# Kernel optimization log

Measured on AMD Instinct MI355X. Metric: run time of the kernel, lower is better.

The kernel has to match this reference:

```python
import jax, jax.numpy as jnp
import numpy as np

N, DIM = 8192, 128

def setup_inputs() -> dict:
    key = jax.random.key(0)
    ks = jax.random.split(key, 9)
    s = 1.0 / np.sqrt(DIM)
    return {
        "x": jax.random.normal(ks[0], (N, DIM), dtype=jnp.float32),
        "Wq": jax.random.uniform(ks[1], (DIM, DIM), jnp.float32, -s, s),
        "bq": jax.random.uniform(ks[2], (DIM,), jnp.float32, -s, s),
        "Wk": jax.random.uniform(ks[3], (DIM, DIM), jnp.float32, -s, s),
        "bk": jax.random.uniform(ks[4], (DIM,), jnp.float32, -s, s),
        "Wv": jax.random.uniform(ks[5], (DIM, DIM), jnp.float32, -s, s),
        "bv": jax.random.uniform(ks[6], (DIM,), jnp.float32, -s, s),
        "Wo": jax.random.uniform(ks[7], (DIM, DIM), jnp.float32, -s, s),
        "bo": jax.random.uniform(ks[8], (DIM,), jnp.float32, -s, s),
    }

def reference(x, Wq, bq, Wk, bk, Wv, bv, Wo, bo):
    # nn.Linear: y = x @ W.T + b
    Q = x @ Wq.T + bq                      # [N, d]
    K = x @ Wk.T + bk                      # [N, d]
    V = x @ Wv.T + bv                      # [N, d]
    scale = 1.0 / jnp.sqrt(jnp.asarray(x.shape[-1], x.dtype))
    scores = (Q @ K.T) * scale             # [N, N] — matches original O(n^2) math
    attn = jax.nn.softmax(scores, axis=-1)
    out = attn @ V                         # [N, d]
    return out @ Wo.T + bo
```

## Files before the change

### kernel.cpp

```cpp
#include <hip/hip_runtime.h>
#include <math.h>


typedef __bf16 bf16x8 __attribute__((ext_vector_type(8)));
typedef float f32x4 __attribute__((ext_vector_type(4)));
typedef unsigned int u32x4 __attribute__((ext_vector_type(4)));
typedef unsigned int u32x2 __attribute__((ext_vector_type(2)));
typedef unsigned short us16;

#define NTOK 8192
#define CHUNKS 8

static constexpr float SCALE_L2E = 0.08838834764831845f * 1.4426950408889634f;

__device__ __forceinline__ unsigned f2bf_u(float x) {
    unsigned u = __builtin_bit_cast(unsigned, x);
    return (u + 0x7FFFu + ((u >> 16) & 1u)) >> 16;
}

__device__ __forceinline__ unsigned pk_bf16(float x, float y) {
    unsigned a = __builtin_bit_cast(unsigned, x) + 0x8000u;
    unsigned b = __builtin_bit_cast(unsigned, y) + 0x8000u;
#if __has_builtin(__builtin_amdgcn_perm)
    return __builtin_amdgcn_perm(b, a, 0x07060302u);
#else
    return (a >> 16) | (b & 0xFFFF0000u);
#endif
}

__device__ __forceinline__ bf16x8 ld_frag(const us16* p) {
    u32x4 u = *reinterpret_cast<const u32x4*>(p);
    return __builtin_bit_cast(bf16x8, u);
}

__global__ __launch_bounds__(256) void cast_all(
    const float* __restrict__ x,
    const float* __restrict__ wq, const float* __restrict__ wk,
    const float* __restrict__ wv, const float* __restrict__ wo,
    us16* __restrict__ xb,
    us16* __restrict__ wqb, us16* __restrict__ wkb,
    us16* __restrict__ wvb, us16* __restrict__ wob)
{
    int b = blockIdx.x;
    const float* src; us16* dst; int off;
    if (b < 512) { src = x; dst = xb; off = b * 2048; }
    else {
        int wi = (b - 512) >> 3, sb = (b - 512) & 7;
        src = wi == 0 ? wq : wi == 1 ? wk : wi == 2 ? wv : wo;
        dst = wi == 0 ? wqb : wi == 1 ? wkb : wi == 2 ? wvb : wob;
        off = sb * 2048;
    }
    int i = off + threadIdx.x * 8;
    f32x4 a = *reinterpret_cast<const f32x4*>(src + i);
    f32x4 c = *reinterpret_cast<const f32x4*>(src + i + 4);
    u32x4 o;
    o[0] = f2bf_u(a[0]) | (f2bf_u(a[1]) << 16);
    o[1] = f2bf_u(a[2]) | (f2bf_u(a[3]) << 16);
    o[2] = f2bf_u(c[0]) | (f2bf_u(c[1]) << 16);
    o[3] = f2bf_u(c[2]) | (f2bf_u(c[3]) << 16);
    *reinterpret_cast<u32x4*>(dst + i) = o;
}

__global__ __launch_bounds__(256) void proj_qkv(
    const us16* __restrict__ xb,
    const us16* __restrict__ wqb, const float* __restrict__ bq,
    const us16* __restrict__ wkb, const float* __restrict__ bk,
    const us16* __restrict__ wvb, const float* __restrict__ bv,
    us16* __restrict__ Qb, us16* __restrict__ Kb, us16* __restrict__ Vt)
{
    int z = blockIdx.x >> 7;
    int tile = blockIdx.x & 127;
    const us16* W = z == 0 ? wqb : z == 1 ? wkb : wvb;
    const float* bias = z == 0 ? bq : z == 1 ? bk : bv;
    float osc = z == 0 ? SCALE_L2E : 1.0f;

    int w = threadIdx.x >> 6, lane = threadIdx.x & 63;
    int quad = lane >> 4, l15 = lane & 15;
    int rbase = tile * 64 + w * 16;

    bf16x8 af[4];
#pragma unroll
    for (int ks = 0; ks < 4; ++ks)
        af[ks] = ld_frag(xb + (rbase + l15) * 128 + ks * 32 + quad * 8);

    f32x4 acc[8];
#pragma unroll
    for (int nt = 0; nt < 8; ++nt) acc[nt] = f32x4{0.f, 0.f, 0.f, 0.f};

#pragma unroll
    for (int nt = 0; nt < 8; ++nt) {
#pragma unroll
        for (int ks = 0; ks < 4; ++ks) {
            bf16x8 bf = ld_frag(W + (nt * 16 + l15) * 128 + ks * 32 + quad * 8);
            acc[nt] = __builtin_amdgcn_mfma_f32_16x16x32_bf16(af[ks], bf, acc[nt], 0, 0, 0);
        }
    }

#pragma unroll
    for (int nt = 0; nt < 8; ++nt) {
        float bb = bias[nt * 16 + l15];
        if (z < 2) {
            us16* Out = z == 0 ? Qb : Kb;
#pragma unroll
            for (int r = 0; r < 4; ++r)
                Out[(rbase + quad * 4 + r) * 128 + nt * 16 + l15] =
                    (us16)f2bf_u((acc[nt][r] + bb) * osc);
        } else {
            int d = nt * 16 + l15, r0 = rbase + quad * 4;
            u32x2 pk;
            pk[0] = f2bf_u(acc[nt][0] + bb) | (f2bf_u(acc[nt][1] + bb) << 16);
            pk[1] = f2bf_u(acc[nt][2] + bb) | (f2bf_u(acc[nt][3] + bb) << 16);
            *reinterpret_cast<u32x2*>(Vt + d * NTOK + r0) = pk;
        }
    }
}

__global__ __launch_bounds__(256, 2) void attn(
    const us16* __restrict__ Qb, const us16* __restrict__ Kb,
    const us16* __restrict__ Vt,
    float* __restrict__ Opart, float* __restrict__ Lpart)
{
    __shared__ us16 ldsK[64 * 136];
    __shared__ us16 ldsV[128 * 72];
    __shared__ us16 ldsP[4][32 * 72];

    int qtile = blockIdx.x >> 3, chunk = blockIdx.x & 7;
    int tid = threadIdx.x, w = tid >> 6, lane = tid & 63;
    int quad = lane >> 4, l15 = lane & 15;
    int qb0 = qtile * 128 + w * 32;

    bf16x8 qf[2][4];
#pragma unroll
    for (int mt = 0; mt < 2; ++mt)
#pragma unroll
        for (int ks = 0; ks < 4; ++ks)
            qf[mt][ks] = ld_frag(Qb + (qb0 + mt * 16 + l15) * 128 + ks * 32 + quad * 8);

    f32x4 o[2][8];
#pragma unroll
    for (int mt = 0; mt < 2; ++mt)
#pragma unroll
        for (int dt = 0; dt < 8; ++dt) o[mt][dt] = f32x4{0.f, 0.f, 0.f, 0.f};

    f32x4 lacc[2];
    lacc[0] = f32x4{0.f, 0.f, 0.f, 0.f};
    lacc[1] = f32x4{0.f, 0.f, 0.f, 0.f};

    u32x4 onesu;
    onesu[0] = onesu[1] = onesu[2] = onesu[3] = 0x3F803F80u;
    bf16x8 ones = __builtin_bit_cast(bf16x8, onesu);

    us16* pw = &ldsP[w][0];

    for (int it = 0; it < 16; ++it) {
        int kk = chunk * 1024 + it * 64;
#pragma unroll
        for (int c = 0; c < 4; ++c) {
            int idx = tid + c * 256;
            int r = idx >> 4, cc = idx & 15;
            *reinterpret_cast<u32x4*>(ldsK + r * 136 + cc * 8) =
                *reinterpret_cast<const u32x4*>(Kb + (kk + r) * 128 + cc * 8);
        }
#pragma unroll
        for (int c = 0; c < 4; ++c) {
            int idx = tid + c * 256;
            int r = idx >> 3, cc = idx & 7;
            *reinterpret_cast<u32x4*>(ldsV + r * 72 + cc * 8) =
                *reinterpret_cast<const u32x4*>(Vt + r * NTOK + kk + cc * 8);
        }
        __syncthreads();

        f32x4 s[2][4];
#pragma unroll
        for (int mt = 0; mt < 2; ++mt)
#pragma unroll
            for (int nt = 0; nt < 4; ++nt) s[mt][nt] = f32x4{0.f, 0.f, 0.f, 0.f};

#pragma unroll
        for (int nt = 0; nt < 4; ++nt) {
#pragma unroll
            for (int ks = 0; ks < 4; ++ks) {
                bf16x8 kf = ld_frag(ldsK + (nt * 16 + l15) * 136 + ks * 32 + quad * 8);
                s[0][nt] = __builtin_amdgcn_mfma_f32_16x16x32_bf16(kf, qf[0][ks], s[0][nt], 0, 0, 0);
                s[1][nt] = __builtin_amdgcn_mfma_f32_16x16x32_bf16(kf, qf[1][ks], s[1][nt], 0, 0, 0);
            }
        }

#pragma unroll
        for (int mt = 0; mt < 2; ++mt) {
#pragma unroll
            for (int nt = 0; nt < 4; ++nt) {
                float p0 = exp2f(s[mt][nt][0]);
                float p1 = exp2f(s[mt][nt][1]);
                float p2 = exp2f(s[mt][nt][2]);
                float p3 = exp2f(s[mt][nt][3]);
                u32x2 wv;
                wv[0] = pk_bf16(p0, p1);
                wv[1] = pk_bf16(p2, p3);
                *reinterpret_cast<u32x2*>(pw + (mt * 16 + l15) * 72 + nt * 16 + quad * 4) = wv;
            }
        }

        asm volatile("s_waitcnt lgkmcnt(0)" ::: "memory");

        bf16x8 afP[2][2];
#pragma unroll
        for (int mt = 0; mt < 2; ++mt)
#pragma unroll
            for (int k2 = 0; k2 < 2; ++k2)
                afP[mt][k2] = ld_frag(pw + (mt * 16 + l15) * 72 + k2 * 32 + quad * 8);

        lacc[0] = __builtin_amdgcn_mfma_f32_16x16x32_bf16(afP[0][0], ones, lacc[0], 0, 0, 0);
        lacc[0] = __builtin_amdgcn_mfma_f32_16x16x32_bf16(afP[0][1], ones, lacc[0], 0, 0, 0);
        lacc[1] = __builtin_amdgcn_mfma_f32_16x16x32_bf16(afP[1][0], ones, lacc[1], 0, 0, 0);
        lacc[1] = __builtin_amdgcn_mfma_f32_16x16x32_bf16(afP[1][1], ones, lacc[1], 0, 0, 0);

#pragma unroll
        for (int dt = 0; dt < 8; ++dt) {
#pragma unroll
            for (int k2 = 0; k2 < 2; ++k2) {
                bf16x8 bv = ld_frag(ldsV + (dt * 16 + l15) * 72 + k2 * 32 + quad * 8);
                o[0][dt] = __builtin_amdgcn_mfma_f32_16x16x32_bf16(afP[0][k2], bv, o[0][dt], 0, 0, 0);
                o[1][dt] = __builtin_amdgcn_mfma_f32_16x16x32_bf16(afP[1][k2], bv, o[1][dt], 0, 0, 0);
            }
        }
        __syncthreads();
    }

#pragma unroll
    for (int mt = 0; mt < 2; ++mt)
#pragma unroll
        for (int dt = 0; dt < 8; ++dt)
#pragma unroll
            for (int r = 0; r < 4; ++r) {
                int row = qb0 + mt * 16 + quad * 4 + r;
                Opart[(size_t)(chunk * NTOK + row) * 128 + dt * 16 + l15] = o[mt][dt][r];
            }
    if (l15 == 0) {
#pragma unroll
        for (int mt = 0; mt < 2; ++mt)
#pragma unroll
            for (int r = 0; r < 4; ++r) {
                int row = qb0 + mt * 16 + quad * 4 + r;
                Lpart[chunk * NTOK + row] = lacc[mt][r];
            }
    }
}

__global__ __launch_bounds__(256) void combine_proj(
    const float* __restrict__ Opart, const float* __restrict__ Lpart,
    const us16* __restrict__ wob, const float* __restrict__ bo,
    float* __restrict__ out)
{
    __shared__ us16 ldsO[64 * 136];
    __shared__ float ldsL[64];

    int tile = blockIdx.x, t = threadIdx.x;
    int r0 = tile * 64;

    if (t < 64) {
        float L = 0.f;
#pragma unroll
        for (int c = 0; c < CHUNKS; ++c) L += Lpart[c * NTOK + r0 + t];
        ldsL[t] = 1.0f / L;
    }

    f32x4 acc[8];
#pragma unroll
    for (int j = 0; j < 8; ++j) acc[j] = f32x4{0.f, 0.f, 0.f, 0.f};

#pragma unroll
    for (int c = 0; c < CHUNKS; ++c) {
        const float* src = Opart + (size_t)(c * NTOK + r0) * 128;
#pragma unroll
        for (int j = 0; j < 8; ++j) {
            f32x4 v = *reinterpret_cast<const f32x4*>(src + j * 1024 + t * 4);
            acc[j] += v;
        }
    }
    __syncthreads();

#pragma unroll
    for (int j = 0; j < 8; ++j) {
        int flat = j * 1024 + t * 4;
        int row = flat >> 7, col = flat & 127;
        float sc = ldsL[row];
        u32x2 wv;
        wv[0] = pk_bf16(acc[j][0] * sc, acc[j][1] * sc);
        wv[1] = pk_bf16(acc[j][2] * sc, acc[j][3] * sc);
        *reinterpret_cast<u32x2*>(ldsO + row * 136 + col) = wv;
    }
    __syncthreads();

    int w = t >> 6, lane = t & 63;
    int quad = lane >> 4, l15 = lane & 15;
    int rloc = w * 16;

    bf16x8 af[4];
#pragma unroll
    for (int ks = 0; ks < 4; ++ks)
        af[ks] = ld_frag(ldsO + (rloc + l15) * 136 + ks * 32 + quad * 8);

    f32x4 acc2[8];
#pragma unroll
    for (int nt = 0; nt < 8; ++nt) acc2[nt] = f32x4{0.f, 0.f, 0.f, 0.f};

#pragma unroll
    for (int nt = 0; nt < 8; ++nt) {
#pragma unroll
        for (int ks = 0; ks < 4; ++ks) {
            bf16x8 bfw = ld_frag(wob + (nt * 16 + l15) * 128 + ks * 32 + quad * 8);
            acc2[nt] = __builtin_amdgcn_mfma_f32_16x16x32_bf16(af[ks], bfw, acc2[nt], 0, 0, 0);
        }
    }
#pragma unroll
    for (int nt = 0; nt < 8; ++nt) {
        float bb = bo[nt * 16 + l15];
#pragma unroll
        for (int r = 0; r < 4; ++r)
            out[(r0 + rloc + quad * 4 + r) * 128 + nt * 16 + l15] = acc2[nt][r] + bb;
    }
}

extern "C" void kernel_launch(void* const* d_in, const int* in_sizes, int n_in,
                              void* d_out, int out_size, void* d_ws, size_t ws_size,
                              hipStream_t stream)
{
    const float* x  = (const float*)d_in[0];
    const float* Wq = (const float*)d_in[1];
    const float* bq = (const float*)d_in[2];
    const float* Wk = (const float*)d_in[3];
    const float* bk = (const float*)d_in[4];
    const float* Wv = (const float*)d_in[5];
    const float* bv = (const float*)d_in[6];
    const float* Wo = (const float*)d_in[7];
    const float* bo = (const float*)d_in[8];

    char* ws = (char*)d_ws;
    const size_t MB = 1024 * 1024;
    us16* xb  = (us16*)(ws + 0 * MB);
    us16* Qb  = (us16*)(ws + 2 * MB);
    us16* Kb  = (us16*)(ws + 4 * MB);
    us16* Vt  = (us16*)(ws + 6 * MB);
    us16* wqb = (us16*)(ws + 8 * MB);
    us16* wkb = (us16*)(ws + 8 * MB + 32 * 1024);
    us16* wvb = (us16*)(ws + 8 * MB + 64 * 1024);
    us16* wob = (us16*)(ws + 8 * MB + 96 * 1024);
    float* Lp = (float*)(ws + 8 * MB + 128 * 1024);
    float* Op = (float*)(ws + 9 * MB);

    cast_all<<<544, 256, 0, stream>>>(x, Wq, Wk, Wv, Wo, xb, wqb, wkb, wvb, wob);
    proj_qkv<<<384, 256, 0, stream>>>(xb, wqb, bq, wkb, bk, wvb, bv, Qb, Kb, Vt);
    attn<<<512, 256, 0, stream>>>(Qb, Kb, Vt, Op, Lp);
    combine_proj<<<128, 256, 0, stream>>>(Op, Lp, wob, bo, (float*)d_out);
}
```

Measured before the change: 149.4 us.

## Fuse casts into projections, swizzle LDS, shrink attention blocks, widen combine grid

Removes the separate cast kernel: the QKV and output projections now load fp32 inputs and weights and convert them to bf16 in registers. The attention kernel drops to 128 threads and 64 query rows per block with twice as many blocks, and replaces padded LDS rows with XOR-swizzled layouts for K, V and P. The combine kernel handles 16 rows per block over 512 blocks, with each wave computing two output column tiles. This saves a launch and the bf16 round trip and raises parallelism, at the cost of redundant fp32 weight loads and conversions in every projection block, and half as many query rows sharing each staged K/V tile.

New measurement: 157.9 us. 1.06x slower.

```diff
diff --git a/kernel.cpp b/kernel.cpp
--- a/kernel.cpp
+++ b/kernel.cpp
@@ -33,44 +33,27 @@
     return __builtin_bit_cast(bf16x8, u);
 }
 
-__global__ __launch_bounds__(256) void cast_all(
-    const float* __restrict__ x,
-    const float* __restrict__ wq, const float* __restrict__ wk,
-    const float* __restrict__ wv, const float* __restrict__ wo,
-    us16* __restrict__ xb,
-    us16* __restrict__ wqb, us16* __restrict__ wkb,
-    us16* __restrict__ wvb, us16* __restrict__ wob)
-{
-    int b = blockIdx.x;
-    const float* src; us16* dst; int off;
-    if (b < 512) { src = x; dst = xb; off = b * 2048; }
-    else {
-        int wi = (b - 512) >> 3, sb = (b - 512) & 7;
-        src = wi == 0 ? wq : wi == 1 ? wk : wi == 2 ? wv : wo;
-        dst = wi == 0 ? wqb : wi == 1 ? wkb : wi == 2 ? wvb : wob;
-        off = sb * 2048;
-    }
-    int i = off + threadIdx.x * 8;
-    f32x4 a = *reinterpret_cast<const f32x4*>(src + i);
-    f32x4 c = *reinterpret_cast<const f32x4*>(src + i + 4);
+__device__ __forceinline__ bf16x8 cvt_frag(const float* p) {
+    f32x4 a = *reinterpret_cast<const f32x4*>(p);
+    f32x4 b = *reinterpret_cast<const f32x4*>(p + 4);
     u32x4 o;
     o[0] = f2bf_u(a[0]) | (f2bf_u(a[1]) << 16);
     o[1] = f2bf_u(a[2]) | (f2bf_u(a[3]) << 16);
-    o[2] = f2bf_u(c[0]) | (f2bf_u(c[1]) << 16);
-    o[3] = f2bf_u(c[2]) | (f2bf_u(c[3]) << 16);
-    *reinterpret_cast<u32x4*>(dst + i) = o;
+    o[2] = f2bf_u(b[0]) | (f2bf_u(b[1]) << 16);
+    o[3] = f2bf_u(b[2]) | (f2bf_u(b[3]) << 16);
+    return __builtin_bit_cast(bf16x8, o);
 }
 
 __global__ __launch_bounds__(256) void proj_qkv(
-    const us16* __restrict__ xb,
-    const us16* __restrict__ wqb, const float* __restrict__ bq,
-    const us16* __restrict__ wkb, const float* __restrict__ bk,
-    const us16* __restrict__ wvb, const float* __restrict__ bv,
+    const float* __restrict__ x,
+    const float* __restrict__ wq, const float* __restrict__ bq,
+    const float* __restrict__ wk, const float* __restrict__ bk,
+    const float* __restrict__ wv, const float* __restrict__ bv,
     us16* __restrict__ Qb, us16* __restrict__ Kb, us16* __restrict__ Vt)
 {
     int z = blockIdx.x >> 7;
     int tile = blockIdx.x & 127;
-    const us16* W = z == 0 ? wqb : z == 1 ? wkb : wvb;
+    const float* W = z == 0 ? wq : z == 1 ? wk : wv;
     const float* bias = z == 0 ? bq : z == 1 ? bk : bv;
     float osc = z == 0 ? SCALE_L2E : 1.0f;
 
@@ -81,7 +64,7 @@
     bf16x8 af[4];
 #pragma unroll
     for (int ks = 0; ks < 4; ++ks)
-        af[ks] = ld_frag(xb + (rbase + l15) * 128 + ks * 32 + quad * 8);
+        af[ks] = cvt_frag(x + (size_t)(rbase + l15) * 128 + ks * 32 + quad * 8);
 
     f32x4 acc[8];
 #pragma unroll
@@ -91,7 +74,7 @@
     for (int nt = 0; nt < 8; ++nt) {
 #pragma unroll
         for (int ks = 0; ks < 4; ++ks) {
-            bf16x8 bf = ld_frag(W + (nt * 16 + l15) * 128 + ks * 32 + quad * 8);
+            bf16x8 bf = cvt_frag(W + (nt * 16 + l15) * 128 + ks * 32 + quad * 8);
             acc[nt] = __builtin_amdgcn_mfma_f32_16x16x32_bf16(af[ks], bf, acc[nt], 0, 0, 0);
         }
     }
@@ -115,19 +98,19 @@
     }
 }
 
-__global__ __launch_bounds__(256, 2) void attn(
+__global__ __launch_bounds__(128, 2) void attn(
     const us16* __restrict__ Qb, const us16* __restrict__ Kb,
     const us16* __restrict__ Vt,
     float* __restrict__ Opart, float* __restrict__ Lpart)
 {
-    __shared__ us16 ldsK[64 * 136];
-    __shared__ us16 ldsV[128 * 72];
-    __shared__ us16 ldsP[4][32 * 72];
+    __shared__ us16 ldsK[64 * 128];
+    __shared__ us16 ldsV[128 * 64];
+    __shared__ us16 ldsP[2][32 * 64];
 
     int qtile = blockIdx.x >> 3, chunk = blockIdx.x & 7;
     int tid = threadIdx.x, w = tid >> 6, lane = tid & 63;
     int quad = lane >> 4, l15 = lane & 15;
-    int qb0 = qtile * 128 + w * 32;
+    int qb0 = qtile * 64 + w * 32;
 
     bf16x8 qf[2][4];
 #pragma unroll
@@ -151,22 +134,21 @@
     bf16x8 ones = __builtin_bit_cast(bf16x8, onesu);
 
     us16* pw = &ldsP[w][0];
+    int pswz = l15 & 7;
 
     for (int it = 0; it < 16; ++it) {
         int kk = chunk * 1024 + it * 64;
 #pragma unroll
-        for (int c = 0; c < 4; ++c) {
-            int idx = tid + c * 256;
-            int r = idx >> 4, cc = idx & 15;
-            *reinterpret_cast<u32x4*>(ldsK + r * 136 + cc * 8) =
-                *reinterpret_cast<const u32x4*>(Kb + (kk + r) * 128 + cc * 8);
-        }
-#pragma unroll
-        for (int c = 0; c < 4; ++c) {
-            int idx = tid + c * 256;
-            int r = idx >> 3, cc = idx & 7;
-            *reinterpret_cast<u32x4*>(ldsV + r * 72 + cc * 8) =
-                *reinterpret_cast<const u32x4*>(Vt + r * NTOK + kk + cc * 8);
+        for (int c = 0; c < 8; ++c) {
+            int idx = tid + c * 128;
+            int kr = idx >> 4, kc = idx & 15;
+            u32x4 kvv = *reinterpret_cast<const u32x4*>(
+                Kb + (size_t)(kk + kr) * 128 + kc * 8);
+            int vr = idx >> 3, vc = idx & 7;
+            u32x4 vvv = *reinterpret_cast<const u32x4*>(
+                Vt + (size_t)vr * NTOK + kk + vc * 8);
+            *reinterpret_cast<u32x4*>(ldsK + kr * 128 + ((kc ^ (kr & 15)) * 8)) = kvv;
+            *reinterpret_cast<u32x4*>(ldsV + vr * 64 + ((vc ^ (vr & 7)) * 8)) = vvv;
         }
         __syncthreads();
 
@@ -180,7 +162,8 @@
         for (int nt = 0; nt < 4; ++nt) {
 #pragma unroll
             for (int ks = 0; ks < 4; ++ks) {
-                bf16x8 kf = ld_frag(ldsK + (nt * 16 + l15) * 136 + ks * 32 + quad * 8);
+                bf16x8 kf = ld_frag(ldsK + (nt * 16 + l15) * 128 +
+                                    ((ks * 4 + quad) ^ l15) * 8);
                 s[0][nt] = __builtin_amdgcn_mfma_f32_16x16x32_bf16(kf, qf[0][ks], s[0][nt], 0, 0, 0);
                 s[1][nt] = __builtin_amdgcn_mfma_f32_16x16x32_bf16(kf, qf[1][ks], s[1][nt], 0, 0, 0);
             }
@@ -197,7 +180,8 @@
                 u32x2 wv;
                 wv[0] = pk_bf16(p0, p1);
                 wv[1] = pk_bf16(p2, p3);
-                *reinterpret_cast<u32x2*>(pw + (mt * 16 + l15) * 72 + nt * 16 + quad * 4) = wv;
+                int cswz = ((nt * 2 + (quad >> 1)) ^ pswz) * 8 + (quad & 1) * 4;
+                *reinterpret_cast<u32x2*>(pw + (mt * 16 + l15) * 64 + cswz) = wv;
             }
         }
 
@@ -208,7 +192,8 @@
         for (int mt = 0; mt < 2; ++mt)
 #pragma unroll
             for (int k2 = 0; k2 < 2; ++k2)
-                afP[mt][k2] = ld_frag(pw + (mt * 16 + l15) * 72 + k2 * 32 + quad * 8);
+                afP[mt][k2] = ld_frag(pw + (mt * 16 + l15) * 64 +
+                                      ((k2 * 4 + quad) ^ pswz) * 8);
 
         lacc[0] = __builtin_amdgcn_mfma_f32_16x16x32_bf16(afP[0][0], ones, lacc[0], 0, 0, 0);
         lacc[0] = __builtin_amdgcn_mfma_f32_16x16x32_bf16(afP[0][1], ones, lacc[0], 0, 0, 0);
@@ -219,7 +204,8 @@
         for (int dt = 0; dt < 8; ++dt) {
 #pragma unroll
             for (int k2 = 0; k2 < 2; ++k2) {
-                bf16x8 bv = ld_frag(ldsV + (dt * 16 + l15) * 72 + k2 * 32 + quad * 8);
+                bf16x8 bv = ld_frag(ldsV + (dt * 16 + l15) * 64 +
+                                    ((k2 * 4 + quad) ^ (l15 & 7)) * 8);
                 o[0][dt] = __builtin_amdgcn_mfma_f32_16x16x32_bf16(afP[0][k2], bv, o[0][dt], 0, 0, 0);
                 o[1][dt] = __builtin_amdgcn_mfma_f32_16x16x32_bf16(afP[1][k2], bv, o[1][dt], 0, 0, 0);
             }
@@ -249,39 +235,37 @@
 
 __global__ __launch_bounds__(256) void combine_proj(
     const float* __restrict__ Opart, const float* __restrict__ Lpart,
-    const us16* __restrict__ wob, const float* __restrict__ bo,
+    const float* __restrict__ Wo, const float* __restrict__ bo,
     float* __restrict__ out)
 {
-    __shared__ us16 ldsO[64 * 136];
-    __shared__ float ldsL[64];
+    __shared__ us16 ldsO[16 * 136];
+    __shared__ float ldsL[16];
 
     int tile = blockIdx.x, t = threadIdx.x;
-    int r0 = tile * 64;
-
-    if (t < 64) {
+    int r0 = tile * 16;
+
+    if (t < 16) {
         float L = 0.f;
 #pragma unroll
         for (int c = 0; c < CHUNKS; ++c) L += Lpart[c * NTOK + r0 + t];
         ldsL[t] = 1.0f / L;
     }
 
-    f32x4 acc[8];
-#pragma unroll
-    for (int j = 0; j < 8; ++j) acc[j] = f32x4{0.f, 0.f, 0.f, 0.f};
+    f32x4 acc[2];
+    acc[0] = f32x4{0.f, 0.f, 0.f, 0.f};
+    acc[1] = f32x4{0.f, 0.f, 0.f, 0.f};
 
 #pragma unroll
     for (int c = 0; c < CHUNKS; ++c) {
         const float* src = Opart + (size_t)(c * NTOK + r0) * 128;
 #pragma unroll
-        for (int j = 0; j < 8; ++j) {
-            f32x4 v = *reinterpret_cast<const f32x4*>(src + j * 1024 + t * 4);
-            acc[j] += v;
-        }
+        for (int j = 0; j < 2; ++j)
+            acc[j] += *reinterpret_cast<const f32x4*>(src + j * 1024 + t * 4);
     }
     __syncthreads();
 
 #pragma unroll
-    for (int j = 0; j < 8; ++j) {
+    for (int j = 0; j < 2; ++j) {
         int flat = j * 1024 + t * 4;
         int row = flat >> 7, col = flat & 127;
         float sc = ldsL[row];
@@ -294,31 +278,32 @@
 
     int w = t >> 6, lane = t & 63;
     int quad = lane >> 4, l15 = lane & 15;
-    int rloc = w * 16;
 
     bf16x8 af[4];
 #pragma unroll
     for (int ks = 0; ks < 4; ++ks)
-        af[ks] = ld_frag(ldsO + (rloc + l15) * 136 + ks * 32 + quad * 8);
-
-    f32x4 acc2[8];
-#pragma unroll
-    for (int nt = 0; nt < 8; ++nt) acc2[nt] = f32x4{0.f, 0.f, 0.f, 0.f};
-
-#pragma unroll
-    for (int nt = 0; nt < 8; ++nt) {
+        af[ks] = ld_frag(ldsO + l15 * 136 + ks * 32 + quad * 8);
+
+    f32x4 acc2[2];
+    acc2[0] = f32x4{0.f, 0.f, 0.f, 0.f};
+    acc2[1] = f32x4{0.f, 0.f, 0.f, 0.f};
+
+#pragma unroll
+    for (int j = 0; j < 2; ++j) {
+        int nt = w * 2 + j;
 #pragma unroll
         for (int ks = 0; ks < 4; ++ks) {
-            bf16x8 bfw = ld_frag(wob + (nt * 16 + l15) * 128 + ks * 32 + quad * 8);
-            acc2[nt] = __builtin_amdgcn_mfma_f32_16x16x32_bf16(af[ks], bfw, acc2[nt], 0, 0, 0);
-        }
-    }
-#pragma unroll
-    for (int nt = 0; nt < 8; ++nt) {
+            bf16x8 bfw = cvt_frag(Wo + (nt * 16 + l15) * 128 + ks * 32 + quad * 8);
+            acc2[j] = __builtin_amdgcn_mfma_f32_16x16x32_bf16(af[ks], bfw, acc2[j], 0, 0, 0);
+        }
+    }
+#pragma unroll
+    for (int j = 0; j < 2; ++j) {
+        int nt = w * 2 + j;
         float bb = bo[nt * 16 + l15];
 #pragma unroll
         for (int r = 0; r < 4; ++r)
-            out[(r0 + rloc + quad * 4 + r) * 128 + nt * 16 + l15] = acc2[nt][r] + bb;
+            out[(r0 + quad * 4 + r) * 128 + nt * 16 + l15] = acc2[j][r] + bb;
     }
 }
 
@@ -338,19 +323,13 @@
 
     char* ws = (char*)d_ws;
     const size_t MB = 1024 * 1024;
-    us16* xb  = (us16*)(ws + 0 * MB);
-    us16* Qb  = (us16*)(ws + 2 * MB);
-    us16* Kb  = (us16*)(ws + 4 * MB);
-    us16* Vt  = (us16*)(ws + 6 * MB);
-    us16* wqb = (us16*)(ws + 8 * MB);
-    us16* wkb = (us16*)(ws + 8 * MB + 32 * 1024);
-    us16* wvb = (us16*)(ws + 8 * MB + 64 * 1024);
-    us16* wob = (us16*)(ws + 8 * MB + 96 * 1024);
-    float* Lp = (float*)(ws + 8 * MB + 128 * 1024);
-    float* Op = (float*)(ws + 9 * MB);
-
-    cast_all<<<544, 256, 0, stream>>>(x, Wq, Wk, Wv, Wo, xb, wqb, wkb, wvb, wob);
-    proj_qkv<<<384, 256, 0, stream>>>(xb, wqb, bq, wkb, bk, wvb, bv, Qb, Kb, Vt);
-    attn<<<512, 256, 0, stream>>>(Qb, Kb, Vt, Op, Lp);
-    combine_proj<<<128, 256, 0, stream>>>(Op, Lp, wob, bo, (float*)d_out);
-}
+    us16* Qb  = (us16*)(ws + 0 * MB);
+    us16* Kb  = (us16*)(ws + 2 * MB);
+    us16* Vt  = (us16*)(ws + 4 * MB);
+    float* Lp = (float*)(ws + 6 * MB);
+    float* Op = (float*)(ws + 8 * MB);
+
+    proj_qkv<<<384, 256, 0, stream>>>(x, Wq, bq, Wk, bk, Wv, bv, Qb, Kb, Vt);
+    attn<<<1024, 128, 0, stream>>>(Qb, Kb, Vt, Op, Lp);
+    combine_proj<<<512, 256, 0, stream>>>(Op, Lp, Wo, bo, (float*)d_out);
+}
```
